# Optimization experiments

Measured on AMD Instinct MI355X. Metric: run time of the kernel, lower is better.

The kernel has to match this reference:

```python
import jax, jax.numpy as jnp
import numpy as np

BS = 4096
D = 256
TAU = 0.5
EPS = 1e-08          # eps added to negative-sum denominator (module arg)
COS_EPS = 1e-08      # nn.CosineSimilarity norm clamp


def setup_inputs() -> dict:
    key = jax.random.key(0)
    k1, k2 = jax.random.split(key)
    zi = jax.random.normal(k1, (BS, D), dtype=jnp.float32)
    zj = jax.random.normal(k2, (BS, D), dtype=jnp.float32)
    return {"zi": zi, "zj": zj}


def reference(zi, zj):
    bs = zi.shape[0]
    n = 2 * bs
    z = jnp.concatenate([zi, zj], axis=0)                       # [2bs, D]
    # cosine similarity = normalized dot products (norms clamped like torch)
    norm = jnp.linalg.norm(z, axis=-1, keepdims=True)
    zn = z / jnp.maximum(norm, COS_EPS)
    sim = jnp.matmul(zn, zn.T) / TAU                            # [2bs, 2bs]
    e = jnp.exp(sim)
    # positive pairs: row i pairs with column (i+bs) mod 2bs
    rows = jnp.arange(n)
    pair = jnp.concatenate([jnp.arange(bs) + bs, jnp.arange(bs)])
    sim_pos = e[rows, pair]                                     # [2bs]
    # negatives: all entries in a row except the diagonal
    sim_neg_sum = e.sum(axis=-1) - jnp.diagonal(e)              # [2bs]
    loss = jnp.mean(-jnp.log(sim_pos / (sim_neg_sum + EPS)))
    return loss
```

## Files before the change

kernel.cpp:

```cpp
#include <hip/hip_runtime.h>
#include <hip/hip_bf16.h>


#define N_ROWS 8192
#define BSZ    4096
#define DIM    256
#define INV_TAU 2.0f
#define EPS_REF 1e-8f
#define COS_EPS 1e-8f
#define NG2     64
#define NTILES  (NG2 * (NG2 + 1) / 2)
#define LSTRIDE 260

typedef __attribute__((ext_vector_type(4))) float f32x4;
typedef long long i64;
typedef union { int4 v; i64 d[2]; } pack16;

__global__ __launch_bounds__(256) void knorm(const float* __restrict__ zi,
                                             const float* __restrict__ zj,
                                             unsigned char* __restrict__ znsw,
                                             float* __restrict__ out) {
    __shared__ float lds[16 * LSTRIDE];
    __shared__ float nrm[16];
    const int rg = blockIdx.x;
    const int t  = threadIdx.x;
    const int w  = t >> 6;
    const int l  = t & 63;
    const int row0 = rg * 16;
    if (rg == 0 && t == 0) out[0] = 0.f;

    #pragma unroll
    for (int s = 0; s < 4; ++s) {
        const int row = s * 4 + w;
        const int r   = row0 + row;
        const float* src = (r < BSZ) ? zi + (size_t)r * DIM + l * 4
                                     : zj + (size_t)(r - BSZ) * DIM + l * 4;
        const float4 v = *(const float4*)src;
        *(float4*)&lds[row * LSTRIDE + l * 4] = v;
        float ss = v.x*v.x + v.y*v.y + v.z*v.z + v.w*v.w;
        #pragma unroll
        for (int off = 32; off >= 1; off >>= 1) ss += __shfl_xor(ss, off);
        if (l == 0) nrm[row] = 1.0f / fmaxf(sqrtf(ss), COS_EPS);
    }
    __syncthreads();

    const int kbp = w, fl = l;
    const int r16 = fl & 15, q = fl >> 4;
    const float inv = nrm[r16];
    int wd[4];
    #pragma unroll
    for (int h = 0; h < 2; ++h) {
        const int kk = (2 * kbp + h) * 32 + q * 8;
        float f[8];
        #pragma unroll
        for (int j = 0; j < 8; ++j) f[j] = lds[r16 * LSTRIDE + kk + j] * inv;
        int a = 0, b = 0;
        a = __builtin_amdgcn_cvt_pk_fp8_f32(f[0], f[1], a, false);
        a = __builtin_amdgcn_cvt_pk_fp8_f32(f[2], f[3], a, true);
        b = __builtin_amdgcn_cvt_pk_fp8_f32(f[4], f[5], b, false);
        b = __builtin_amdgcn_cvt_pk_fp8_f32(f[6], f[7], b, true);
        wd[h * 2] = a; wd[h * 2 + 1] = b;
    }
    *(int4*)(znsw + ((size_t)(rg * 4 + kbp) * 64 + fl) * 16) =
        make_int4(wd[0], wd[1], wd[2], wd[3]);
}

__global__ __launch_bounds__(256, 3) void kgemm(const unsigned char* __restrict__ znsw,
                                                float* __restrict__ P,
                                                float* __restrict__ selfdot,
                                                float* __restrict__ pairdot) {
    __shared__ __align__(16) unsigned char pan[32768];
    const int w = threadIdx.x >> 6;
    const int l = threadIdx.x & 63;

    const int t = blockIdx.x;
    int Gi = (int)((129.0f - sqrtf(16641.0f - 8.0f * (float)t)) * 0.5f);
    while ((Gi + 1) * (129 - (Gi + 1)) / 2 <= t) ++Gi;
    while (Gi * (129 - Gi) / 2 > t) --Gi;
    const int Gj = Gi + (t - Gi * (129 - Gi) / 2);

    const char* srcA = (const char*)znsw + (size_t)Gi * 32768;
    #pragma unroll
    for (int sub = 0; sub < 8; ++sub) {
        const int off = sub * 4096 + w * 1024;
        __builtin_amdgcn_global_load_lds(
            (const __attribute__((address_space(1))) void*)(srcA + off + l * 16),
            (__attribute__((address_space(3))) void*)(&pan[off]), 16, 0, 0);
    }

    const int rh = w >> 1, ch = w & 1;
    const char* Ap    = (const char*)&pan[0] + rh * 16384 + l * 16;
    const char* bbase = (const char*)znsw + (size_t)Gj * 32768 + ch * 16384 + l * 16;

    pack16 Bcur[4], Bnxt[4];
    #pragma unroll
    for (int nt = 0; nt < 4; ++nt)
        Bcur[nt].v = *(const int4*)(bbase + nt * 4096);

    f32x4 acc[4][4];
    #pragma unroll
    for (int mt = 0; mt < 4; ++mt)
        #pragma unroll
        for (int nt = 0; nt < 4; ++nt)
            acc[mt][nt] = (f32x4){0.f, 0.f, 0.f, 0.f};

    __syncthreads();

    #pragma unroll
    for (int kbp = 0; kbp < 4; ++kbp) {
        if (kbp < 3) {
            #pragma unroll
            for (int nt = 0; nt < 4; ++nt)
                Bnxt[nt].v = *(const int4*)(bbase + nt * 4096 + (kbp + 1) * 1024);
        }
        pack16 Afr[4];
        #pragma unroll
        for (int mt = 0; mt < 4; ++mt)
            Afr[mt].v = *(const int4*)(Ap + mt * 4096 + kbp * 1024);
        #pragma unroll
        for (int mt = 0; mt < 4; ++mt)
            #pragma unroll
            for (int nt = 0; nt < 4; ++nt) {
                acc[mt][nt] = __builtin_amdgcn_mfma_f32_16x16x32_fp8_fp8(
                    Afr[mt].d[0], Bcur[nt].d[0], acc[mt][nt], 0, 0, 0);
                acc[mt][nt] = __builtin_amdgcn_mfma_f32_16x16x32_fp8_fp8(
                    Afr[mt].d[1], Bcur[nt].d[1], acc[mt][nt], 0, 0, 0);
            }
        #pragma unroll
        for (int nt = 0; nt < 4; ++nt) Bcur[nt] = Bnxt[nt];
    }

    const int c = l & 15, q = l >> 4;
    const int rsel = c - 4 * q;
    const bool vld = (rsel >= 0) && (rsel < 4);

    if ((Gi == Gj || Gj == Gi + 32) && rh == ch) {
        float dv[4];
        #pragma unroll
        for (int mt = 0; mt < 4; ++mt) {
            float d = acc[mt][mt][0];
            #pragma unroll
            for (int r = 1; r < 4; ++r)
                if (rsel == r) d = acc[mt][mt][r];
            dv[mt] = d;
        }
        if (vld) {
            float* dst = (Gi == Gj) ? selfdot : pairdot;
            #pragma unroll
            for (int mt = 0; mt < 4; ++mt)
                dst[Gi * 128 + rh * 64 + mt * 16 + c] = dv[mt];
        }
    }

    #pragma unroll
    for (int mt = 0; mt < 4; ++mt)
        #pragma unroll
        for (int nt = 0; nt < 4; ++nt)
            #pragma unroll
            for (int r = 0; r < 4; ++r)
                acc[mt][nt][r] = __expf(acc[mt][nt][r] * INV_TAU);

    float rs[4][4];
    #pragma unroll
    for (int mt = 0; mt < 4; ++mt)
        #pragma unroll
        for (int r = 0; r < 4; ++r)
            rs[mt][r] = acc[mt][0][r] + acc[mt][1][r] + acc[mt][2][r] + acc[mt][3][r];
    #pragma unroll
    for (int off = 1; off <= 8; off <<= 1)
        #pragma unroll
        for (int mt = 0; mt < 4; ++mt)
            #pragma unroll
            for (int r = 0; r < 4; ++r)
                rs[mt][r] += __shfl_xor(rs[mt][r], off);
    if (c == 0) {
        #pragma unroll
        for (int mt = 0; mt < 4; ++mt) {
            const f32x4 o4 = (f32x4){rs[mt][0], rs[mt][1], rs[mt][2], rs[mt][3]};
            __builtin_nontemporal_store(o4,
                (f32x4*)&P[(size_t)(Gj * 2 + ch) * N_ROWS + Gi * 128 + rh * 64 + mt * 16 + q * 4]);
        }
    }

    if (Gi != Gj) {
        float cs[4];
        #pragma unroll
        for (int nt = 0; nt < 4; ++nt) {
            float s = 0.f;
            #pragma unroll
            for (int mt = 0; mt < 4; ++mt)
                #pragma unroll
                for (int r = 0; r < 4; ++r)
                    s += acc[mt][nt][r];
            s += __shfl_xor(s, 16);
            s += __shfl_xor(s, 32);
            cs[nt] = s;
        }
        if (q == 0) {
            #pragma unroll
            for (int nt = 0; nt < 4; ++nt)
                __builtin_nontemporal_store(cs[nt],
                    &P[(size_t)(Gi * 2 + rh) * N_ROWS + Gj * 128 + ch * 64 + nt * 16 + c]);
        }
    }
}

__global__ __launch_bounds__(256) void kfinal(const float* __restrict__ P,
                                              const float* __restrict__ selfdot,
                                              const float* __restrict__ pairdot,
                                              float* __restrict__ out) {
    const int l = threadIdx.x & 63;
    const int w = threadIdx.x >> 6;
    const int row = blockIdx.x * 64 + l;
    float s = 0.f;
    #pragma unroll
    for (int st = 0; st < 32; ++st)
        s += P[(size_t)(w * 32 + st) * N_ROWS + row];
    __shared__ float wsum[4][64];
    wsum[w][l] = s;
    __syncthreads();
    if (w == 0) {
        const float tot = wsum[0][l] + wsum[1][l] + wsum[2][l] + wsum[3][l];
        const float selfe = __expf(selfdot[row] * INV_TAU);
        const float pd    = pairdot[(row < BSZ) ? row : row - BSZ];
        float loss = logf(tot - selfe + EPS_REF) - pd * INV_TAU;
        #pragma unroll
        for (int off = 32; off >= 1; off >>= 1) loss += __shfl_xor(loss, off);
        if (l == 0) atomicAdd(out, loss * (1.0f / (float)N_ROWS));
    }
}

extern "C" void kernel_launch(void* const* d_in, const int* in_sizes, int n_in,
                              void* d_out, int out_size, void* d_ws, size_t ws_size,
                              hipStream_t stream) {
    const float* zi = (const float*)d_in[0];
    const float* zj = (const float*)d_in[1];
    float* out = (float*)d_out;

    char* ws = (char*)d_ws;
    unsigned char* znsw = (unsigned char*)ws;
    float* P       = (float*)(ws + 2 * 1024 * 1024);
    float* selfdot = (float*)(ws + 6 * 1024 * 1024);
    float* pairdot = (float*)(ws + 6 * 1024 * 1024 + 32 * 1024);

    knorm <<<N_ROWS / 16, 256, 0, stream>>>(zi, zj, znsw, out);
    kgemm <<<NTILES, 256, 0, stream>>>(znsw, P, selfdot, pairdot);
    kfinal<<<N_ROWS / 64, 256, 0, stream>>>(P, selfdot, pairdot, out);
}
```

Measured before the change: 86.43 us.

## Replace partial-sum matrix with atomic row sums, DPP reductions, deeper B prefetch

Drops the 4MB partial-sum buffer P. The GEMM tiles now atomically add their row and column exp-sums directly into an 8192-entry rowsum array, which knorm zeroes, so kfinal only reads one value per row. Row reductions use DPP row_shr operations instead of shfl_xor. B fragments are prefetched two k-steps ahead with a double buffer. The atomic contention on rowsum (many tiles hitting the same rows) may offset the traffic saved, and float atomics make the summation order nondeterministic.

Result: slower. 98.45 us (+13.9%).

```diff
diff --git a/kernel.cpp b/kernel.cpp
--- a/kernel.cpp
+++ b/kernel.cpp
@@ -16,9 +16,18 @@
 typedef long long i64;
 typedef union { int4 v; i64 d[2]; } pack16;
 
+__device__ __forceinline__ float red16(float x) {
+    x += __int_as_float(__builtin_amdgcn_update_dpp(0, __float_as_int(x), 0x121, 0xf, 0xf, false));
+    x += __int_as_float(__builtin_amdgcn_update_dpp(0, __float_as_int(x), 0x122, 0xf, 0xf, false));
+    x += __int_as_float(__builtin_amdgcn_update_dpp(0, __float_as_int(x), 0x124, 0xf, 0xf, false));
+    x += __int_as_float(__builtin_amdgcn_update_dpp(0, __float_as_int(x), 0x128, 0xf, 0xf, false));
+    return x;
+}
+
 __global__ __launch_bounds__(256) void knorm(const float* __restrict__ zi,
                                              const float* __restrict__ zj,
                                              unsigned char* __restrict__ znsw,
+                                             float* __restrict__ rowsum,
                                              float* __restrict__ out) {
     __shared__ float lds[16 * LSTRIDE];
     __shared__ float nrm[16];
@@ -28,6 +37,7 @@
     const int l  = t & 63;
     const int row0 = rg * 16;
     if (rg == 0 && t == 0) out[0] = 0.f;
+    if (t < 16) rowsum[row0 + t] = 0.f;
 
     #pragma unroll
     for (int s = 0; s < 4; ++s) {
@@ -66,7 +76,7 @@
 }
 
 __global__ __launch_bounds__(256, 3) void kgemm(const unsigned char* __restrict__ znsw,
-                                                float* __restrict__ P,
+                                                float* __restrict__ rowsum,
                                                 float* __restrict__ selfdot,
                                                 float* __restrict__ pairdot) {
     __shared__ __align__(16) unsigned char pan[32768];
@@ -92,10 +102,11 @@
     const char* Ap    = (const char*)&pan[0] + rh * 16384 + l * 16;
     const char* bbase = (const char*)znsw + (size_t)Gj * 32768 + ch * 16384 + l * 16;
 
-    pack16 Bcur[4], Bnxt[4];
-    #pragma unroll
-    for (int nt = 0; nt < 4; ++nt)
-        Bcur[nt].v = *(const int4*)(bbase + nt * 4096);
+    pack16 Bbuf[2][4];
+    #pragma unroll
+    for (int nt = 0; nt < 4; ++nt) Bbuf[0][nt].v = *(const int4*)(bbase + nt * 4096);
+    #pragma unroll
+    for (int nt = 0; nt < 4; ++nt) Bbuf[1][nt].v = *(const int4*)(bbase + nt * 4096 + 1024);
 
     f32x4 acc[4][4];
     #pragma unroll
@@ -108,15 +119,19 @@
 
     #pragma unroll
     for (int kbp = 0; kbp < 4; ++kbp) {
-        if (kbp < 3) {
-            #pragma unroll
-            for (int nt = 0; nt < 4; ++nt)
-                Bnxt[nt].v = *(const int4*)(bbase + nt * 4096 + (kbp + 1) * 1024);
-        }
+        const int cur = kbp & 1;
         pack16 Afr[4];
         #pragma unroll
         for (int mt = 0; mt < 4; ++mt)
             Afr[mt].v = *(const int4*)(Ap + mt * 4096 + kbp * 1024);
+        pack16 Bcur[4];
+        #pragma unroll
+        for (int nt = 0; nt < 4; ++nt) Bcur[nt] = Bbuf[cur][nt];
+        if (kbp < 2) {
+            #pragma unroll
+            for (int nt = 0; nt < 4; ++nt)
+                Bbuf[cur][nt].v = *(const int4*)(bbase + nt * 4096 + (kbp + 2) * 1024);
+        }
         #pragma unroll
         for (int mt = 0; mt < 4; ++mt)
             #pragma unroll
@@ -126,8 +141,6 @@
                 acc[mt][nt] = __builtin_amdgcn_mfma_f32_16x16x32_fp8_fp8(
                     Afr[mt].d[1], Bcur[nt].d[1], acc[mt][nt], 0, 0, 0);
             }
-        #pragma unroll
-        for (int nt = 0; nt < 4; ++nt) Bcur[nt] = Bnxt[nt];
     }
 
     const int c = l & 15, q = l >> 4;
@@ -165,21 +178,14 @@
     for (int mt = 0; mt < 4; ++mt)
         #pragma unroll
         for (int r = 0; r < 4; ++r)
-            rs[mt][r] = acc[mt][0][r] + acc[mt][1][r] + acc[mt][2][r] + acc[mt][3][r];
-    #pragma unroll
-    for (int off = 1; off <= 8; off <<= 1)
+            rs[mt][r] = red16(acc[mt][0][r] + acc[mt][1][r] + acc[mt][2][r] + acc[mt][3][r]);
+    if (c == 0) {
+        const int rbase = Gi * 128 + rh * 64 + q * 4;
         #pragma unroll
         for (int mt = 0; mt < 4; ++mt)
             #pragma unroll
             for (int r = 0; r < 4; ++r)
-                rs[mt][r] += __shfl_xor(rs[mt][r], off);
-    if (c == 0) {
-        #pragma unroll
-        for (int mt = 0; mt < 4; ++mt) {
-            const f32x4 o4 = (f32x4){rs[mt][0], rs[mt][1], rs[mt][2], rs[mt][3]};
-            __builtin_nontemporal_store(o4,
-                (f32x4*)&P[(size_t)(Gj * 2 + ch) * N_ROWS + Gi * 128 + rh * 64 + mt * 16 + q * 4]);
-        }
+                atomicAdd(&rowsum[rbase + mt * 16 + r], rs[mt][r]);
     }
 
     if (Gi != Gj) {
@@ -197,37 +203,30 @@
             cs[nt] = s;
         }
         if (q == 0) {
+            const int cbase = Gj * 128 + ch * 64 + c;
             #pragma unroll
             for (int nt = 0; nt < 4; ++nt)
-                __builtin_nontemporal_store(cs[nt],
-                    &P[(size_t)(Gi * 2 + rh) * N_ROWS + Gj * 128 + ch * 64 + nt * 16 + c]);
-        }
-    }
-}
-
-__global__ __launch_bounds__(256) void kfinal(const float* __restrict__ P,
+                atomicAdd(&rowsum[cbase + nt * 16], cs[nt]);
+        }
+    }
+}
+
+__global__ __launch_bounds__(256) void kfinal(const float* __restrict__ rowsum,
                                               const float* __restrict__ selfdot,
                                               const float* __restrict__ pairdot,
                                               float* __restrict__ out) {
-    const int l = threadIdx.x & 63;
-    const int w = threadIdx.x >> 6;
-    const int row = blockIdx.x * 64 + l;
-    float s = 0.f;
-    #pragma unroll
-    for (int st = 0; st < 32; ++st)
-        s += P[(size_t)(w * 32 + st) * N_ROWS + row];
-    __shared__ float wsum[4][64];
-    wsum[w][l] = s;
+    const int i = blockIdx.x * 256 + threadIdx.x;
+    const float s     = rowsum[i];
+    const float selfe = __expf(selfdot[i] * INV_TAU);
+    const float pd    = pairdot[(i < BSZ) ? i : i - BSZ];
+    float loss = logf(s - selfe + EPS_REF) - pd * INV_TAU;
+    #pragma unroll
+    for (int off = 32; off >= 1; off >>= 1) loss += __shfl_xor(loss, off);
+    __shared__ float wsum[4];
+    if ((threadIdx.x & 63) == 0) wsum[threadIdx.x >> 6] = loss;
     __syncthreads();
-    if (w == 0) {
-        const float tot = wsum[0][l] + wsum[1][l] + wsum[2][l] + wsum[3][l];
-        const float selfe = __expf(selfdot[row] * INV_TAU);
-        const float pd    = pairdot[(row < BSZ) ? row : row - BSZ];
-        float loss = logf(tot - selfe + EPS_REF) - pd * INV_TAU;
-        #pragma unroll
-        for (int off = 32; off >= 1; off >>= 1) loss += __shfl_xor(loss, off);
-        if (l == 0) atomicAdd(out, loss * (1.0f / (float)N_ROWS));
-    }
+    if (threadIdx.x == 0)
+        atomicAdd(out, (wsum[0] + wsum[1] + wsum[2] + wsum[3]) * (1.0f / (float)N_ROWS));
 }
 
 extern "C" void kernel_launch(void* const* d_in, const int* in_sizes, int n_in,
@@ -239,11 +238,11 @@
 
     char* ws = (char*)d_ws;
     unsigned char* znsw = (unsigned char*)ws;
-    float* P       = (float*)(ws + 2 * 1024 * 1024);
-    float* selfdot = (float*)(ws + 6 * 1024 * 1024);
-    float* pairdot = (float*)(ws + 6 * 1024 * 1024 + 32 * 1024);
-
-    knorm <<<N_ROWS / 16, 256, 0, stream>>>(zi, zj, znsw, out);
-    kgemm <<<NTILES, 256, 0, stream>>>(znsw, P, selfdot, pairdot);
-    kfinal<<<N_ROWS / 64, 256, 0, stream>>>(P, selfdot, pairdot, out);
-}
+    float* rowsum  = (float*)(ws + 2 * 1024 * 1024);
+    float* selfdot = (float*)(ws + 2 * 1024 * 1024 + 32 * 1024);
+    float* pairdot = (float*)(ws + 2 * 1024 * 1024 + 64 * 1024);
+
+    knorm <<<N_ROWS / 16, 256, 0, stream>>>(zi, zj, znsw, rowsum, out);
+    kgemm <<<NTILES, 256, 0, stream>>>(znsw, rowsum, selfdot, pairdot);
+    kfinal<<<N_ROWS / 256, 256, 0, stream>>>(rowsum, selfdot, pairdot, out);
+}
```
